# Performance work log

Measured on AMD Instinct MI355X. Metric: run time of the kernel, lower is better.

Reference implementation:

```python
import jax, jax.numpy as jnp
import numpy as np

HIDDEN = 2048
HEADS = 16
HEAD_DIM = HIDDEN // HEADS  # 128
SCALE = 1.0 / np.sqrt(HEAD_DIM).astype(np.float32)


def setup_inputs() -> dict:
    key = jax.random.key(0)
    k1, k2, k3, k4, k5 = jax.random.split(key, 5)
    B, QL = 8, 1024
    NB, BS = 32, 128  # num_blocks, block_size -> kv_len = 4096
    query = jax.random.normal(k1, (B, QL, HIDDEN), dtype=jnp.float32)
    kv_k = jax.random.normal(k2, (NB, BS, HIDDEN), dtype=jnp.float32)
    kv_v = jax.random.normal(k3, (NB, BS, HIDDEN), dtype=jnp.float32)
    # nn.Linear(bias=False) weights: y = x @ W.T
    Wq = jax.random.normal(k4, (HIDDEN, HIDDEN), dtype=jnp.float32) * (1.0 / np.sqrt(HIDDEN))
    Wo = jax.random.normal(k5, (HIDDEN, HIDDEN), dtype=jnp.float32) * (1.0 / np.sqrt(HIDDEN))
    return {"query": query, "kv_k": kv_k, "kv_v": kv_v, "Wq": Wq, "Wo": Wo}


def reference(query, kv_k, kv_v, Wq, Wo):
    # query: [B, QL, H*D]; kv_k/kv_v: [NB, BS, H*D] (shared across batch,
    # NOT re-projected in the paged path, matching the torch module).
    B, QL, _ = query.shape
    NB, BS, _ = kv_k.shape
    KV = NB * BS
    Q = (query @ Wq.T).reshape(B, QL, HEADS, HEAD_DIM)          # bqhd
    K = kv_k.reshape(KV, HEADS, HEAD_DIM)                        # khd
    V = kv_v.reshape(KV, HEADS, HEAD_DIM)
    # Blockwise online-softmax over equal blocks == one stable softmax over kv.
    scores = jnp.einsum("bqhd,khd->bhqk", Q, K) * SCALE          # [B,H,QL,KV]
    attn = jax.nn.softmax(scores, axis=-1)
    out = jnp.einsum("bhqk,khd->bqhd", attn, V).reshape(B, QL, HIDDEN)
    return out @ Wo.T
```

## Files before the change

### kernel.cpp

```cpp
#include <hip/hip_runtime.h>

#define HIDDEN 2048
#define HEADS 16
#define HDIM 128
#define BQ 8
#define QLEN 1024
#define KVLEN 4096
#define MROWS (BQ * QLEN)

typedef __bf16 bf16x8 __attribute__((ext_vector_type(8)));
typedef float f32x4 __attribute__((ext_vector_type(4)));
typedef unsigned short u16;
typedef u16 u16x8 __attribute__((ext_vector_type(8)));
typedef float f32x8v __attribute__((ext_vector_type(8)));

__device__ __forceinline__ void async_ld16(const void* g, void* l) {
  __builtin_amdgcn_global_load_lds(
      (const __attribute__((address_space(1))) void*)g,
      (__attribute__((address_space(3))) void*)l, 16, 0, 0);
}

__global__ void convert_bf16(const float* __restrict__ src, u16* __restrict__ dst,
                             long n) {
  long base = ((long)blockIdx.x * blockDim.x + threadIdx.x) * 8;
  long stride = (long)gridDim.x * blockDim.x * 8;
  for (long i = base; i < n; i += stride) {
    f32x8v s = *(const f32x8v*)(src + i);
    bf16x8 o;
#pragma unroll
    for (int j = 0; j < 8; j++) o[j] = (__bf16)s[j];
    *(bf16x8*)(dst + i) = o;
  }
}

__global__ __launch_bounds__(256) void transpose_v(const float* __restrict__ V,
                                                   u16* __restrict__ Vt) {
  __shared__ __bf16 T[128][129];
  const int kv0 = blockIdx.x * 128;
  const int h = blockIdx.y;
  const int tid = threadIdx.x;
#pragma unroll
  for (int p = 0; p < 8; p++) {
    int idx = p * 2048 + tid * 8;
    int r = idx >> 7, c = idx & 127;
    f32x8v s = *(const f32x8v*)(V + (size_t)(kv0 + r) * HIDDEN + h * HDIM + c);
#pragma unroll
    for (int j = 0; j < 8; j++) T[r][c + j] = (__bf16)s[j];
  }
  __syncthreads();
#pragma unroll
  for (int p = 0; p < 8; p++) {
    int idx = p * 2048 + tid * 8;
    int d = idx >> 7, kv = idx & 127;
    bf16x8 o;
#pragma unroll
    for (int j = 0; j < 8; j++) o[j] = T[kv + j][d];
    *(bf16x8*)(Vt + ((size_t)h * HDIM + d) * KVLEN + kv0 + kv) = o;
  }
}

__global__ __launch_bounds__(256) void gemm_bt(
    const u16* __restrict__ A, const u16* __restrict__ Bt, void* __restrict__ C,
    int M, int N, int K, int outf) {
  __shared__ __align__(16) u16 Asm[4 * 128 * 8];
  __shared__ __align__(16) u16 Bsm[4 * 128 * 8];
  const int tid = threadIdx.x;
  const int wid = tid >> 6, lane = tid & 63;
  const int quad = lane >> 4, l15 = lane & 15;
  const int wm = wid >> 1, wn = wid & 1;
  const int lin = blockIdx.y * gridDim.x + blockIdx.x;
  const int cpx = (gridDim.x * gridDim.y) >> 3;
  const int swz = (lin & 7) * cpx + (lin >> 3);
  const int by = swz / gridDim.x;
  const int bx = swz - by * gridDim.x;
  const int row0 = by * 128;
  const int col0 = bx * 128;

  f32x4 acc[4][4];
#pragma unroll
  for (int i = 0; i < 4; i++)
#pragma unroll
    for (int j = 0; j < 4; j++) acc[i][j] = (f32x4){0.f, 0.f, 0.f, 0.f};

  for (int k0 = 0; k0 < K; k0 += 32) {
    __syncthreads();
#pragma unroll
    for (int i = 0; i < 4; i++) {
      int seg = wid + 4 * i;
      int isB = seg >> 3;
      int s = seg & 7;
      int q = s >> 1, hv = s & 1;
      const u16* gsrc = isB ? Bt : A;
      int grow = (isB ? col0 : row0) + hv * 64 + lane;
      const u16* g = gsrc + (size_t)grow * K + (k0 + q * 8);
      u16* l = (isB ? Bsm : Asm) + (q * 128 + hv * 64) * 8;
      async_ld16(g, l);
    }
    __syncthreads();
    bf16x8 af[4], bfr[4];
#pragma unroll
    for (int mt = 0; mt < 4; mt++)
      af[mt] = *(const bf16x8*)(Asm + (quad * 128 + wm * 64 + mt * 16 + l15) * 8);
#pragma unroll
    for (int nt = 0; nt < 4; nt++)
      bfr[nt] = *(const bf16x8*)(Bsm + (quad * 128 + wn * 64 + nt * 16 + l15) * 8);
#pragma unroll
    for (int mt = 0; mt < 4; mt++)
#pragma unroll
      for (int nt = 0; nt < 4; nt++)
        acc[mt][nt] = __builtin_amdgcn_mfma_f32_16x16x32_bf16(af[mt], bfr[nt], acc[mt][nt], 0, 0, 0);
  }

#pragma unroll
  for (int mt = 0; mt < 4; mt++)
#pragma unroll
    for (int r = 0; r < 4; r++) {
      int row = row0 + wm * 64 + mt * 16 + quad * 4 + r;
#pragma unroll
      for (int nt = 0; nt < 4; nt++) {
        int col = col0 + wn * 64 + nt * 16 + l15;
        if (outf) {
          ((float*)C)[(size_t)row * N + col] = acc[mt][nt][r];
        } else {
          ((__bf16*)C)[(size_t)row * N + col] = (__bf16)acc[mt][nt][r];
        }
      }
    }
}

__global__ __launch_bounds__(512, 4) void attn(
    const u16* __restrict__ Q,
    const u16* __restrict__ Kv,
    const u16* __restrict__ Vt,
    u16* __restrict__ O) {
  __shared__ __align__(16) u16 KVb[16 * 1024];
  __shared__ __align__(16) __bf16 Pb[128 * 136];
  const int tid = threadIdx.x;
  const int wid = tid >> 6, lane = tid & 63;
  const int quad = lane >> 4, l15 = lane & 15;
  const int lin = blockIdx.x + (blockIdx.y << 3) + (blockIdx.z << 7);
  const int swz = ((lin & 7) << 7) + (lin >> 3);
  const int h = swz >> 6, b = (swz >> 3) & 7, qt = swz & 7;
  const int qrow0 = b * QLEN + qt * 128;
  const int hcol = h * HDIM;
  const float cexp = 0.08838834764831845f * 1.4426950408889634f;

  bf16x8 qf[4];
#pragma unroll
  for (int ks = 0; ks < 4; ks++) {
    int row = qrow0 + wid * 16 + l15;
    qf[ks] = *(const bf16x8*)(Q + (size_t)row * HIDDEN + hcol + ks * 32 + quad * 8);
  }

  f32x4 o[8];
#pragma unroll
  for (int dt = 0; dt < 8; dt++) o[dt] = (f32x4){0.f, 0.f, 0.f, 0.f};
  float mrun[4], lrun[4];
#pragma unroll
  for (int r = 0; r < 4; r++) { mrun[r] = -INFINITY; lrun[r] = 0.f; }

  for (int kv0 = 0; kv0 < KVLEN; kv0 += 128) {
    __syncthreads();
#pragma unroll
    for (int i = 0; i < 4; i++) {
      int seg = wid + 8 * i;
      int ch = seg >> 1, sh = seg & 1;
      int kvr = kv0 + sh * 64 + lane;
      const u16* g = Kv + (size_t)kvr * HIDDEN + hcol + ch * 8;
      async_ld16(g, KVb + (ch * 128 + sh * 64) * 8);
    }
    __syncthreads();

    f32x4 sc[8];
#pragma unroll
    for (int nt = 0; nt < 8; nt++) sc[nt] = (f32x4){0.f, 0.f, 0.f, 0.f};
#pragma unroll
    for (int ks = 0; ks < 4; ks++) {
#pragma unroll
      for (int hf = 0; hf < 2; hf++) {
        bf16x8 kf[4];
#pragma unroll
        for (int j = 0; j < 4; j++)
          kf[j] = *(const bf16x8*)(KVb + ((ks * 4 + quad) * 128 + (hf * 4 + j) * 16 + l15) * 8);
#pragma unroll
        for (int j = 0; j < 4; j++)
          sc[hf * 4 + j] = __builtin_amdgcn_mfma_f32_16x16x32_bf16(qf[ks], kf[j], sc[hf * 4 + j], 0, 0, 0);
      }
    }
    __syncthreads();

#pragma unroll
    for (int i = 0; i < 4; i++) {
      int seg = wid + 8 * i;
      int ch = seg >> 1, dh = seg & 1;
      int d = dh * 64 + lane;
      const u16* g = Vt + ((size_t)hcol + d) * KVLEN + kv0 + ch * 8;
      async_ld16(g, KVb + (ch * 128 + dh * 64) * 8);
    }

    float mx[4];
#pragma unroll
    for (int r = 0; r < 4; r++) {
      float m = sc[0][r];
#pragma unroll
      for (int nt = 1; nt < 8; nt++) m = fmaxf(m, sc[nt][r]);
#pragma unroll
      for (int off = 1; off < 16; off <<= 1) m = fmaxf(m, __shfl_xor(m, off, 64));
      mx[r] = m;
    }
    float gmax = fmaxf(fmaxf(mx[0] - mrun[0], mx[1] - mrun[1]),
                       fmaxf(mx[2] - mrun[2], mx[3] - mrun[3]));
    if (__any(gmax > 8.f)) {
#pragma unroll
      for (int r = 0; r < 4; r++) {
        float mn = fmaxf(mrun[r], mx[r]);
        float al = __builtin_amdgcn_exp2f((mrun[r] - mn) * cexp);
        mrun[r] = mn;
        lrun[r] *= al;
#pragma unroll
        for (int dt = 0; dt < 8; dt++) o[dt][r] *= al;
      }
    }
#pragma unroll
    for (int r = 0; r < 4; r++) {
      float mc = mrun[r] * cexp;
      float ps = 0.f;
#pragma unroll
      for (int nt = 0; nt < 8; nt++) {
        float p = __builtin_amdgcn_exp2f(sc[nt][r] * cexp - mc);
        sc[nt][r] = p;
        ps += p;
      }
#pragma unroll
      for (int off = 1; off < 16; off <<= 1) ps += __shfl_xor(ps, off, 64);
      lrun[r] += ps;
    }

#pragma unroll
    for (int nt = 0; nt < 8; nt++)
#pragma unroll
      for (int r = 0; r < 4; r++) {
        int prow = wid * 16 + quad * 4 + r;
        Pb[prow * 136 + nt * 16 + l15] = (__bf16)sc[nt][r];
      }
    __syncthreads();

#pragma unroll
    for (int ks = 0; ks < 4; ks++) {
      bf16x8 pf = *(const bf16x8*)(Pb + (wid * 16 + l15) * 136 + ks * 32 + quad * 8);
#pragma unroll
      for (int hf = 0; hf < 2; hf++) {
        bf16x8 vf[4];
#pragma unroll
        for (int j = 0; j < 4; j++)
          vf[j] = *(const bf16x8*)(KVb + ((ks * 4 + quad) * 128 + (hf * 4 + j) * 16 + l15) * 8);
#pragma unroll
        for (int j = 0; j < 4; j++)
          o[hf * 4 + j] = __builtin_amdgcn_mfma_f32_16x16x32_bf16(pf, vf[j], o[hf * 4 + j], 0, 0, 0);
      }
    }
  }

#pragma unroll
  for (int r = 0; r < 4; r++) {
    float inv = 1.0f / lrun[r];
    int row = qrow0 + wid * 16 + quad * 4 + r;
#pragma unroll
    for (int dt = 0; dt < 8; dt++) {
      int col = hcol + dt * 16 + l15;
      ((__bf16*)O)[(size_t)row * HIDDEN + col] = (__bf16)(o[dt][r] * inv);
    }
  }
}

extern "C" void kernel_launch(void* const* d_in, const int* in_sizes, int n_in,
                              void* d_out, int out_size, void* d_ws, size_t ws_size,
                              hipStream_t stream) {
  const float* query = (const float*)d_in[0];
  const float* kv_k  = (const float*)d_in[1];
  const float* kv_v  = (const float*)d_in[2];
  const float* Wq    = (const float*)d_in[3];
  const float* Wo    = (const float*)d_in[4];
  float* out = (float*)d_out;

  const long NQ = (long)MROWS * HIDDEN;
  const long NK = (long)KVLEN * HIDDEN;
  const long NW = (long)HIDDEN * HIDDEN;

  dim3 blk(256);

  u16* convQ  = (u16*)d_ws;
  u16* convK  = convQ + NQ;
  u16* Vtb    = convK + NK;
  u16* convWq = Vtb + NK;
  u16* convWo = convWq + NW;
  u16* Qws    = convWo + NW;
  u16* Ows    = convQ;

  convert_bf16<<<dim3((NQ / 8 + 255) / 256), blk, 0, stream>>>(query, convQ,  NQ);
  convert_bf16<<<dim3((NK / 8 + 255) / 256), blk, 0, stream>>>(kv_k,  convK,  NK);
  transpose_v<<<dim3(KVLEN / 128, HEADS), blk, 0, stream>>>(kv_v, Vtb);
  convert_bf16<<<dim3((NW / 8 + 255) / 256), blk, 0, stream>>>(Wq,    convWq, NW);
  convert_bf16<<<dim3((NW / 8 + 255) / 256), blk, 0, stream>>>(Wo,    convWo, NW);

  gemm_bt<<<dim3(HIDDEN / 128, MROWS / 128), blk, 0, stream>>>(convQ, convWq, Qws, MROWS, HIDDEN, HIDDEN, 0);
  attn<<<dim3(QLEN / 128, HEADS, BQ), dim3(512), 0, stream>>>(Qws, convK, Vtb, Ows);
  gemm_bt<<<dim3(HIDDEN / 128, MROWS / 128), blk, 0, stream>>>(Ows, convWo, out, MROWS, HIDDEN, HIDDEN, 1);
}
```

Baseline: 956.1 us.

## Double GEMM K-step per barrier and halve attention P staging buffer

The projection GEMM now loads a 64-wide K slice per iteration and runs two MFMA sub-steps between barriers, which halves the synchronization and loop overhead per unit of work. The attention kernel writes the probability tile to shared memory in two 64-column halves through a smaller buffer, cutting LDS use from about 34KB to about 18KB for P. This is meant to raise occupancy. The second half is written without a barrier after the first half is consumed. Each wave only reads rows it wrote itself, so this is likely safe but depends on wave-local ordering.

Measured after the change: 879.3 us. -8.0%, faster.

```diff
diff --git a/kernel.cpp b/kernel.cpp
--- a/kernel.cpp
+++ b/kernel.cpp
@@ -62,8 +62,8 @@
 __global__ __launch_bounds__(256) void gemm_bt(
     const u16* __restrict__ A, const u16* __restrict__ Bt, void* __restrict__ C,
     int M, int N, int K, int outf) {
-  __shared__ __align__(16) u16 Asm[4 * 128 * 8];
-  __shared__ __align__(16) u16 Bsm[4 * 128 * 8];
+  __shared__ __align__(16) u16 Asm[8 * 128 * 8];
+  __shared__ __align__(16) u16 Bsm[8 * 128 * 8];
   const int tid = threadIdx.x;
   const int wid = tid >> 6, lane = tid & 63;
   const int quad = lane >> 4, l15 = lane & 15;
@@ -82,13 +82,13 @@
 #pragma unroll
     for (int j = 0; j < 4; j++) acc[i][j] = (f32x4){0.f, 0.f, 0.f, 0.f};
 
-  for (int k0 = 0; k0 < K; k0 += 32) {
-    __syncthreads();
-#pragma unroll
-    for (int i = 0; i < 4; i++) {
+  for (int k0 = 0; k0 < K; k0 += 64) {
+    __syncthreads();
+#pragma unroll
+    for (int i = 0; i < 8; i++) {
       int seg = wid + 4 * i;
-      int isB = seg >> 3;
-      int s = seg & 7;
+      int isB = seg >> 4;
+      int s = seg & 15;
       int q = s >> 1, hv = s & 1;
       const u16* gsrc = isB ? Bt : A;
       int grow = (isB ? col0 : row0) + hv * 64 + lane;
@@ -97,18 +97,21 @@
       async_ld16(g, l);
     }
     __syncthreads();
-    bf16x8 af[4], bfr[4];
-#pragma unroll
-    for (int mt = 0; mt < 4; mt++)
-      af[mt] = *(const bf16x8*)(Asm + (quad * 128 + wm * 64 + mt * 16 + l15) * 8);
-#pragma unroll
-    for (int nt = 0; nt < 4; nt++)
-      bfr[nt] = *(const bf16x8*)(Bsm + (quad * 128 + wn * 64 + nt * 16 + l15) * 8);
-#pragma unroll
-    for (int mt = 0; mt < 4; mt++)
+#pragma unroll
+    for (int kk = 0; kk < 2; kk++) {
+      bf16x8 af[4], bfr[4];
+#pragma unroll
+      for (int mt = 0; mt < 4; mt++)
+        af[mt] = *(const bf16x8*)(Asm + ((kk * 4 + quad) * 128 + wm * 64 + mt * 16 + l15) * 8);
 #pragma unroll
       for (int nt = 0; nt < 4; nt++)
-        acc[mt][nt] = __builtin_amdgcn_mfma_f32_16x16x32_bf16(af[mt], bfr[nt], acc[mt][nt], 0, 0, 0);
+        bfr[nt] = *(const bf16x8*)(Bsm + ((kk * 4 + quad) * 128 + wn * 64 + nt * 16 + l15) * 8);
+#pragma unroll
+      for (int mt = 0; mt < 4; mt++)
+#pragma unroll
+        for (int nt = 0; nt < 4; nt++)
+          acc[mt][nt] = __builtin_amdgcn_mfma_f32_16x16x32_bf16(af[mt], bfr[nt], acc[mt][nt], 0, 0, 0);
+    }
   }
 
 #pragma unroll
@@ -134,7 +137,7 @@
     const u16* __restrict__ Vt,
     u16* __restrict__ O) {
   __shared__ __align__(16) u16 KVb[16 * 1024];
-  __shared__ __align__(16) __bf16 Pb[128 * 136];
+  __shared__ __align__(16) __bf16 Pb[128 * 72];
   const int tid = threadIdx.x;
   const int wid = tid >> 6, lane = tid & 63;
   const int quad = lane >> 4, l15 = lane & 15;
@@ -237,23 +240,46 @@
     }
 
 #pragma unroll
-    for (int nt = 0; nt < 8; nt++)
+    for (int nt = 0; nt < 4; nt++)
 #pragma unroll
       for (int r = 0; r < 4; r++) {
         int prow = wid * 16 + quad * 4 + r;
-        Pb[prow * 136 + nt * 16 + l15] = (__bf16)sc[nt][r];
-      }
-    __syncthreads();
-
-#pragma unroll
-    for (int ks = 0; ks < 4; ks++) {
-      bf16x8 pf = *(const bf16x8*)(Pb + (wid * 16 + l15) * 136 + ks * 32 + quad * 8);
+        Pb[prow * 72 + nt * 16 + l15] = (__bf16)sc[nt][r];
+      }
+    __syncthreads();
+
+#pragma unroll
+    for (int ks2 = 0; ks2 < 2; ks2++) {
+      bf16x8 pf = *(const bf16x8*)(Pb + (wid * 16 + l15) * 72 + ks2 * 32 + quad * 8);
 #pragma unroll
       for (int hf = 0; hf < 2; hf++) {
         bf16x8 vf[4];
 #pragma unroll
         for (int j = 0; j < 4; j++)
-          vf[j] = *(const bf16x8*)(KVb + ((ks * 4 + quad) * 128 + (hf * 4 + j) * 16 + l15) * 8);
+          vf[j] = *(const bf16x8*)(KVb + ((ks2 * 4 + quad) * 128 + (hf * 4 + j) * 16 + l15) * 8);
+#pragma unroll
+        for (int j = 0; j < 4; j++)
+          o[hf * 4 + j] = __builtin_amdgcn_mfma_f32_16x16x32_bf16(pf, vf[j], o[hf * 4 + j], 0, 0, 0);
+      }
+    }
+
+#pragma unroll
+    for (int nt = 0; nt < 4; nt++)
+#pragma unroll
+      for (int r = 0; r < 4; r++) {
+        int prow = wid * 16 + quad * 4 + r;
+        Pb[prow * 72 + nt * 16 + l15] = (__bf16)sc[4 + nt][r];
+      }
+
+#pragma unroll
+    for (int ks2 = 0; ks2 < 2; ks2++) {
+      bf16x8 pf = *(const bf16x8*)(Pb + (wid * 16 + l15) * 72 + ks2 * 32 + quad * 8);
+#pragma unroll
+      for (int hf = 0; hf < 2; hf++) {
+        bf16x8 vf[4];
+#pragma unroll
+        for (int j = 0; j < 4; j++)
+          vf[j] = *(const bf16x8*)(KVb + (((2 + ks2) * 4 + quad) * 128 + (hf * 4 + j) * 16 + l15) * 8);
 #pragma unroll
         for (int j = 0; j < 4; j++)
           o[hf * 4 + j] = __builtin_amdgcn_mfma_f32_16x16x32_bf16(pf, vf[j], o[hf * 4 + j], 0, 0, 0);
```

## Double-buffer GEMM tiles and prefetch next K tile during attention softmax

Applied to the files above, without the earlier changes.

The projection GEMM now uses two LDS buffers, so the next K-slice is loaded while the current one feeds the MFMAs, and one barrier per step is dropped. The attention kernel splits the shared K/V buffer into separate K and V buffers, so the V tile and the next K tile load during softmax instead of after a barrier. The P tile is staged through a smaller LDS buffer in 32-column chunks, interleaved with the PV MFMAs. s_setprio raises wave priority around the MFMA sections. Costs are more LDS use, which may reduce occupancy, and more reliance on barrier placement for correct async-load completion.

Result: faster. 889.1 us (-7.0%).

```diff
diff --git a/kernel.cpp b/kernel.cpp
--- a/kernel.cpp
+++ b/kernel.cpp
@@ -62,8 +62,8 @@
 __global__ __launch_bounds__(256) void gemm_bt(
     const u16* __restrict__ A, const u16* __restrict__ Bt, void* __restrict__ C,
     int M, int N, int K, int outf) {
-  __shared__ __align__(16) u16 Asm[4 * 128 * 8];
-  __shared__ __align__(16) u16 Bsm[4 * 128 * 8];
+  __shared__ __align__(16) u16 Asm[2 * 4 * 128 * 8];
+  __shared__ __align__(16) u16 Bsm[2 * 4 * 128 * 8];
   const int tid = threadIdx.x;
   const int wid = tid >> 6, lane = tid & 63;
   const int quad = lane >> 4, l15 = lane & 15;
@@ -76,14 +76,7 @@
   const int row0 = by * 128;
   const int col0 = bx * 128;
 
-  f32x4 acc[4][4];
-#pragma unroll
-  for (int i = 0; i < 4; i++)
-#pragma unroll
-    for (int j = 0; j < 4; j++) acc[i][j] = (f32x4){0.f, 0.f, 0.f, 0.f};
-
-  for (int k0 = 0; k0 < K; k0 += 32) {
-    __syncthreads();
+  auto stage = [&](int buf, int k0) {
 #pragma unroll
     for (int i = 0; i < 4; i++) {
       int seg = wid + 4 * i;
@@ -93,22 +86,36 @@
       const u16* gsrc = isB ? Bt : A;
       int grow = (isB ? col0 : row0) + hv * 64 + lane;
       const u16* g = gsrc + (size_t)grow * K + (k0 + q * 8);
-      u16* l = (isB ? Bsm : Asm) + (q * 128 + hv * 64) * 8;
+      u16* l = (isB ? Bsm : Asm) + buf * 4096 + (q * 128 + hv * 64) * 8;
       async_ld16(g, l);
     }
-    __syncthreads();
+  };
+
+  f32x4 acc[4][4];
+#pragma unroll
+  for (int i = 0; i < 4; i++)
+#pragma unroll
+    for (int j = 0; j < 4; j++) acc[i][j] = (f32x4){0.f, 0.f, 0.f, 0.f};
+
+  stage(0, 0);
+  __syncthreads();
+  int cur = 0;
+  for (int k0 = 0; k0 < K; k0 += 32) {
+    if (k0 + 32 < K) stage(cur ^ 1, k0 + 32);
     bf16x8 af[4], bfr[4];
 #pragma unroll
     for (int mt = 0; mt < 4; mt++)
-      af[mt] = *(const bf16x8*)(Asm + (quad * 128 + wm * 64 + mt * 16 + l15) * 8);
+      af[mt] = *(const bf16x8*)(Asm + cur * 4096 + (quad * 128 + wm * 64 + mt * 16 + l15) * 8);
 #pragma unroll
     for (int nt = 0; nt < 4; nt++)
-      bfr[nt] = *(const bf16x8*)(Bsm + (quad * 128 + wn * 64 + nt * 16 + l15) * 8);
+      bfr[nt] = *(const bf16x8*)(Bsm + cur * 4096 + (quad * 128 + wn * 64 + nt * 16 + l15) * 8);
 #pragma unroll
     for (int mt = 0; mt < 4; mt++)
 #pragma unroll
       for (int nt = 0; nt < 4; nt++)
         acc[mt][nt] = __builtin_amdgcn_mfma_f32_16x16x32_bf16(af[mt], bfr[nt], acc[mt][nt], 0, 0, 0);
+    __syncthreads();
+    cur ^= 1;
   }
 
 #pragma unroll
@@ -133,8 +140,9 @@
     const u16* __restrict__ Kv,
     const u16* __restrict__ Vt,
     u16* __restrict__ O) {
-  __shared__ __align__(16) u16 KVb[16 * 1024];
-  __shared__ __align__(16) __bf16 Pb[128 * 136];
+  __shared__ __align__(16) u16 Kb[16 * 1024];
+  __shared__ __align__(16) u16 Vb[16 * 1024];
+  __shared__ __align__(16) __bf16 Pb[128 * 40];
   const int tid = threadIdx.x;
   const int wid = tid >> 6, lane = tid & 63;
   const int quad = lane >> 4, l15 = lane & 15;
@@ -145,58 +153,69 @@
   const int hcol = h * HDIM;
   const float cexp = 0.08838834764831845f * 1.4426950408889634f;
 
-  bf16x8 qf[4];
-#pragma unroll
-  for (int ks = 0; ks < 4; ks++) {
-    int row = qrow0 + wid * 16 + l15;
-    qf[ks] = *(const bf16x8*)(Q + (size_t)row * HIDDEN + hcol + ks * 32 + quad * 8);
-  }
-
-  f32x4 o[8];
-#pragma unroll
-  for (int dt = 0; dt < 8; dt++) o[dt] = (f32x4){0.f, 0.f, 0.f, 0.f};
-  float mrun[4], lrun[4];
-#pragma unroll
-  for (int r = 0; r < 4; r++) { mrun[r] = -INFINITY; lrun[r] = 0.f; }
-
-  for (int kv0 = 0; kv0 < KVLEN; kv0 += 128) {
-    __syncthreads();
+  auto stageK = [&](int kv0) {
 #pragma unroll
     for (int i = 0; i < 4; i++) {
       int seg = wid + 8 * i;
       int ch = seg >> 1, sh = seg & 1;
       int kvr = kv0 + sh * 64 + lane;
-      const u16* g = Kv + (size_t)kvr * HIDDEN + hcol + ch * 8;
-      async_ld16(g, KVb + (ch * 128 + sh * 64) * 8);
-    }
-    __syncthreads();
-
-    f32x4 sc[8];
-#pragma unroll
-    for (int nt = 0; nt < 8; nt++) sc[nt] = (f32x4){0.f, 0.f, 0.f, 0.f};
-#pragma unroll
-    for (int ks = 0; ks < 4; ks++) {
-#pragma unroll
-      for (int hf = 0; hf < 2; hf++) {
-        bf16x8 kf[4];
-#pragma unroll
-        for (int j = 0; j < 4; j++)
-          kf[j] = *(const bf16x8*)(KVb + ((ks * 4 + quad) * 128 + (hf * 4 + j) * 16 + l15) * 8);
-#pragma unroll
-        for (int j = 0; j < 4; j++)
-          sc[hf * 4 + j] = __builtin_amdgcn_mfma_f32_16x16x32_bf16(qf[ks], kf[j], sc[hf * 4 + j], 0, 0, 0);
-      }
-    }
-    __syncthreads();
-
+      async_ld16(Kv + (size_t)kvr * HIDDEN + hcol + ch * 8,
+                 Kb + (ch * 128 + sh * 64) * 8);
+    }
+  };
+  auto stageV = [&](int kv0) {
 #pragma unroll
     for (int i = 0; i < 4; i++) {
       int seg = wid + 8 * i;
       int ch = seg >> 1, dh = seg & 1;
       int d = dh * 64 + lane;
-      const u16* g = Vt + ((size_t)hcol + d) * KVLEN + kv0 + ch * 8;
-      async_ld16(g, KVb + (ch * 128 + dh * 64) * 8);
-    }
+      async_ld16(Vt + ((size_t)hcol + d) * KVLEN + kv0 + ch * 8,
+                 Vb + (ch * 128 + dh * 64) * 8);
+    }
+  };
+
+  bf16x8 qf[4];
+#pragma unroll
+  for (int ks = 0; ks < 4; ks++) {
+    int row = qrow0 + wid * 16 + l15;
+    qf[ks] = *(const bf16x8*)(Q + (size_t)row * HIDDEN + hcol + ks * 32 + quad * 8);
+  }
+
+  f32x4 o[8];
+#pragma unroll
+  for (int dt = 0; dt < 8; dt++) o[dt] = (f32x4){0.f, 0.f, 0.f, 0.f};
+  float mrun[4], lrun[4];
+#pragma unroll
+  for (int r = 0; r < 4; r++) { mrun[r] = -INFINITY; lrun[r] = 0.f; }
+
+  stageK(0);
+  __syncthreads();
+
+  for (int t = 0; t < KVLEN / 128; t++) {
+    const int kv0 = t << 7;
+
+    f32x4 sc[8];
+#pragma unroll
+    for (int nt = 0; nt < 8; nt++) sc[nt] = (f32x4){0.f, 0.f, 0.f, 0.f};
+    __builtin_amdgcn_s_setprio(1);
+#pragma unroll
+    for (int ks = 0; ks < 4; ks++) {
+#pragma unroll
+      for (int hf = 0; hf < 2; hf++) {
+        bf16x8 kf[4];
+#pragma unroll
+        for (int j = 0; j < 4; j++)
+          kf[j] = *(const bf16x8*)(Kb + ((ks * 4 + quad) * 128 + (hf * 4 + j) * 16 + l15) * 8);
+#pragma unroll
+        for (int j = 0; j < 4; j++)
+          sc[hf * 4 + j] = __builtin_amdgcn_mfma_f32_16x16x32_bf16(qf[ks], kf[j], sc[hf * 4 + j], 0, 0, 0);
+      }
+    }
+    __builtin_amdgcn_s_setprio(0);
+    __syncthreads();
+
+    stageV(kv0);
+    if (t + 1 < KVLEN / 128) stageK(kv0 + 128);
 
     float mx[4];
 #pragma unroll
@@ -237,28 +256,36 @@
     }
 
 #pragma unroll
-    for (int nt = 0; nt < 8; nt++)
-#pragma unroll
-      for (int r = 0; r < 4; r++) {
-        int prow = wid * 16 + quad * 4 + r;
-        Pb[prow * 136 + nt * 16 + l15] = (__bf16)sc[nt][r];
-      }
+    for (int nt = 0; nt < 2; nt++)
+#pragma unroll
+      for (int r = 0; r < 4; r++)
+        Pb[(wid * 16 + quad * 4 + r) * 40 + nt * 16 + l15] = (__bf16)sc[nt][r];
+
     __syncthreads();
 
-#pragma unroll
-    for (int ks = 0; ks < 4; ks++) {
-      bf16x8 pf = *(const bf16x8*)(Pb + (wid * 16 + l15) * 136 + ks * 32 + quad * 8);
+    __builtin_amdgcn_s_setprio(1);
+#pragma unroll
+    for (int qq = 0; qq < 4; qq++) {
+      bf16x8 pf = *(const bf16x8*)(Pb + (wid * 16 + l15) * 40 + quad * 8);
 #pragma unroll
       for (int hf = 0; hf < 2; hf++) {
         bf16x8 vf[4];
 #pragma unroll
         for (int j = 0; j < 4; j++)
-          vf[j] = *(const bf16x8*)(KVb + ((ks * 4 + quad) * 128 + (hf * 4 + j) * 16 + l15) * 8);
+          vf[j] = *(const bf16x8*)(Vb + ((qq * 4 + quad) * 128 + (hf * 4 + j) * 16 + l15) * 8);
 #pragma unroll
         for (int j = 0; j < 4; j++)
           o[hf * 4 + j] = __builtin_amdgcn_mfma_f32_16x16x32_bf16(pf, vf[j], o[hf * 4 + j], 0, 0, 0);
       }
-    }
+      if (qq < 3) {
+#pragma unroll
+        for (int nt = 0; nt < 2; nt++)
+#pragma unroll
+          for (int r = 0; r < 4; r++)
+            Pb[(wid * 16 + quad * 4 + r) * 40 + nt * 16 + l15] = (__bf16)sc[2 * (qq + 1) + nt][r];
+      }
+    }
+    __builtin_amdgcn_s_setprio(0);
   }
 
 #pragma unroll
```
